# Kernel tuning notes

Measured on AMD Instinct MI355X. Metric: run time of the kernel, lower is better.

The kernel has to match this reference:

```python
import jax, jax.numpy as jnp
import numpy as np
from jax import lax

C_RED = 32
IN_CH = 256
BN_EPS = 1e-5
NORM_EPS = 1e-6


def setup_inputs() -> dict:
    key = jax.random.key(0)
    ks = jax.random.split(key, 5)
    B, H, W = 16, 64, 64
    x = jax.random.normal(ks[0], (B, IN_CH, H, W), dtype=jnp.float32)
    w_reduce = jax.random.normal(ks[1], (C_RED, IN_CH), dtype=jnp.float32) * 0.05
    bn_gamma = jnp.ones((C_RED,), dtype=jnp.float32)
    bn_beta = jnp.zeros((C_RED,), dtype=jnp.float32)
    bn_mean = jax.random.normal(ks[2], (C_RED,), dtype=jnp.float32) * 0.1
    bn_var = jax.random.uniform(ks[3], (C_RED,), dtype=jnp.float32, minval=0.5, maxval=1.5)
    # depthwise 3x3 kernel, OIHW with I=1 (groups == channels)
    dw_weight = jax.random.normal(ks[4], (C_RED, 1, 3, 3), dtype=jnp.float32) * 0.1
    scale = jnp.ones((C_RED,), dtype=jnp.float32)
    return {"x": x, "w_reduce": w_reduce, "bn_gamma": bn_gamma, "bn_beta": bn_beta,
            "bn_mean": bn_mean, "bn_var": bn_var, "dw_weight": dw_weight, "scale": scale}


def _l2_normalize(t):
    # F.normalize(p=2, dim=1, eps=1e-6): divide by max(||t||_2, eps) along channel dim
    n = jnp.sqrt(jnp.sum(t * t, axis=1, keepdims=True))
    return t / jnp.maximum(n, NORM_EPS)


def reference(x, w_reduce, bn_gamma, bn_beta, bn_mean, bn_var, dw_weight, scale):
    # 1x1 reduce conv (no bias)
    z = jnp.einsum('bihw,oi->bohw', x, w_reduce)
    # BatchNorm2d (inference: running stats)
    inv = bn_gamma / jnp.sqrt(bn_var + BN_EPS)
    z = z * inv[None, :, None, None] + (bn_beta - bn_mean * inv)[None, :, None, None]
    z = jax.nn.relu(z)
    # SpiralTwist: depthwise 3x3 conv (SAME) then per-channel scale
    z_tw = lax.conv_general_dilated(
        z, dw_weight, window_strides=(1, 1), padding='SAME',
        feature_group_count=C_RED,
        dimension_numbers=('NCHW', 'OIHW', 'NCHW'))
    z_tw = z_tw * scale[None, :, None, None]
    z_norm = _l2_normalize(z)
    z_tw_norm = _l2_normalize(z_tw)
    # upper-triangular channel pairs (i <= j)
    idx_i, idx_j = np.triu_indices(C_RED, k=0)
    pair = z_norm[:, idx_i] * z_tw_norm[:, idx_j]  # [B, C*(C+1)/2, H, W]
    return jnp.concatenate([z_norm, pair], axis=1)
```

## Files before the change

kernel.cpp:

```cpp
#include <hip/hip_runtime.h>
#include <hip/hip_bf16.h>
#include <stdint.h>

#define HW   4096
#define CIN  256
#define CR   32
#define COUT 560

__global__ __launch_bounds__(256) void k_conv1x1(
    const float* __restrict__ x,
    const float* __restrict__ wr,
    const float* __restrict__ gamma,
    const float* __restrict__ beta,
    const float* __restrict__ mean,
    const float* __restrict__ var,
    float* __restrict__ z)
{
    __shared__ __align__(16) float wlds[CR * CIN];
    const int tid = threadIdx.x;
    {
        const float4* wr4 = (const float4*)wr;
        float4* wl4 = (float4*)wlds;
        #pragma unroll
        for (int k = 0; k < 8; ++k) wl4[tid + k * 256] = wr4[tid + k * 256];
    }
    __syncthreads();

    const int og   = tid >> 6;
    const int lane = tid & 63;
    const int g0 = blockIdx.x * 256 + lane * 4;
    const int b = g0 >> 12;
    const int p = g0 & 4095;
    const float* xb = x + ((((size_t)b) * CIN) << 12) + p;
    const int ob = og * 8;

    float4 acc[8];
    #pragma unroll
    for (int o = 0; o < 8; ++o) acc[o] = make_float4(0.f, 0.f, 0.f, 0.f);

    for (int i4 = 0; i4 < 64; ++i4) {
        float4 xv0 = *(const float4*)(xb + ((size_t)(i4 * 4 + 0) << 12));
        float4 xv1 = *(const float4*)(xb + ((size_t)(i4 * 4 + 1) << 12));
        float4 xv2 = *(const float4*)(xb + ((size_t)(i4 * 4 + 2) << 12));
        float4 xv3 = *(const float4*)(xb + ((size_t)(i4 * 4 + 3) << 12));
        #pragma unroll
        for (int o = 0; o < 8; ++o) {
            float4 wv = *(const float4*)&wlds[(ob + o) * 256 + i4 * 4];
            acc[o].x = fmaf(xv0.x, wv.x, acc[o].x);
            acc[o].y = fmaf(xv0.y, wv.x, acc[o].y);
            acc[o].z = fmaf(xv0.z, wv.x, acc[o].z);
            acc[o].w = fmaf(xv0.w, wv.x, acc[o].w);
            acc[o].x = fmaf(xv1.x, wv.y, acc[o].x);
            acc[o].y = fmaf(xv1.y, wv.y, acc[o].y);
            acc[o].z = fmaf(xv1.z, wv.y, acc[o].z);
            acc[o].w = fmaf(xv1.w, wv.y, acc[o].w);
            acc[o].x = fmaf(xv2.x, wv.z, acc[o].x);
            acc[o].y = fmaf(xv2.y, wv.z, acc[o].y);
            acc[o].z = fmaf(xv2.z, wv.z, acc[o].z);
            acc[o].w = fmaf(xv2.w, wv.z, acc[o].w);
            acc[o].x = fmaf(xv3.x, wv.w, acc[o].x);
            acc[o].y = fmaf(xv3.y, wv.w, acc[o].y);
            acc[o].z = fmaf(xv3.z, wv.w, acc[o].z);
            acc[o].w = fmaf(xv3.w, wv.w, acc[o].w);
        }
    }

    #pragma unroll
    for (int o = 0; o < 8; ++o) {
        const int oc = ob + o;
        const float inv = gamma[oc] / sqrtf(var[oc] + 1e-5f);
        const float bia = beta[oc] - mean[oc] * inv;
        float4 r;
        r.x = fmaxf(fmaf(acc[o].x, inv, bia), 0.f);
        r.y = fmaxf(fmaf(acc[o].y, inv, bia), 0.f);
        r.z = fmaxf(fmaf(acc[o].z, inv, bia), 0.f);
        r.w = fmaxf(fmaf(acc[o].w, inv, bia), 0.f);
        *(float4*)(z + ((((size_t)b) * CR + oc) << 12) + p) = r;
    }
}

__global__ __launch_bounds__(256) void k_twist(
    const float* __restrict__ z,
    const float* __restrict__ dww,
    const float* __restrict__ scl,
    float* __restrict__ out)
{
    __shared__ float dml[CR * 9];
    __shared__ float sc[CR];
    const int tid = threadIdx.x;
    for (int t = tid; t < CR * 9; t += 256) dml[t] = dww[t];
    if (tid < CR) sc[tid] = scl[tid];
    __syncthreads();

    const int g = blockIdx.x * 256 + tid;
    const int b = g >> 12;
    const int p = g & 4095;
    const int h = p >> 6;
    const int w = p & 63;
    const float* zb = z + (((size_t)b * CR) << 12);

    float zc[CR], tw[CR];
    float s1 = 0.f, s2 = 0.f;
    #pragma unroll
    for (int c = 0; c < CR; ++c) {
        const float* zp = zb + ((size_t)c << 12);
        float acc = 0.f;
        float center = 0.f;
        #pragma unroll
        for (int dy = 0; dy < 3; ++dy) {
            const int hy = h + dy - 1;
            const bool rok = ((unsigned)hy) < 64u;
            #pragma unroll
            for (int dx = 0; dx < 3; ++dx) {
                const int wx = w + dx - 1;
                const bool ok = rok && (((unsigned)wx) < 64u);
                float v = 0.f;
                if (ok) v = zp[(hy << 6) + wx];
                if (dy == 1 && dx == 1) center = v;
                acc = fmaf(v, dml[c * 9 + dy * 3 + dx], acc);
            }
        }
        const float t = acc * sc[c];
        zc[c] = center;
        tw[c] = t;
        s1 = fmaf(center, center, s1);
        s2 = fmaf(t, t, s2);
    }
    const float rn1 = 1.0f / fmaxf(sqrtf(s1), 1e-6f);
    const float rn2 = 1.0f / fmaxf(sqrtf(s2), 1e-6f);
    #pragma unroll
    for (int c = 0; c < CR; ++c) { zc[c] *= rn1; tw[c] *= rn2; }

    float* op = out + (((size_t)b * COUT) << 12) + p;
    #pragma unroll
    for (int c = 0; c < CR; ++c) op[(size_t)c << 12] = zc[c];

    float* pp = op + ((size_t)CR << 12);
    #pragma unroll
    for (int i = 0; i < CR; ++i) {
        const float a = zc[i];
        #pragma unroll
        for (int j = i; j < CR; ++j) {
            *pp = a * tw[j];
            pp += HW;
        }
    }
}

extern "C" void kernel_launch(void* const* d_in, const int* in_sizes, int n_in,
                              void* d_out, int out_size, void* d_ws, size_t ws_size,
                              hipStream_t stream) {
    const float* x     = (const float*)d_in[0];
    const float* wr    = (const float*)d_in[1];
    const float* gamma = (const float*)d_in[2];
    const float* beta  = (const float*)d_in[3];
    const float* mean  = (const float*)d_in[4];
    const float* var   = (const float*)d_in[5];
    const float* dww   = (const float*)d_in[6];
    const float* scl   = (const float*)d_in[7];
    float* z = (float*)d_ws;
    float* out = (float*)d_out;

    hipLaunchKernelGGL(k_conv1x1, dim3(256), dim3(256), 0, stream,
                       x, wr, gamma, beta, mean, var, z);
    hipLaunchKernelGGL(k_twist, dim3(256), dim3(256), 0, stream,
                       z, dww, scl, out);
}
```

Baseline: 276.1 us.

## Split conv and twist work across more blocks with channel-group wave partitioning

The 1x1 conv now has each thread handle one pixel instead of four, with weights read from global memory through wave-uniform scalar loads in place of the LDS copy, and the grid grows fourfold. The twist kernel splits its 32 channels across four waves, reduces the norm partial sums through LDS, stages normalized values in LDS, and interleaves output rows across the waves. This is meant to raise occupancy and parallelism, since the old 256-block grids underfilled the GPU. In exchange it adds LDS traffic and barriers, and the conv kernel loses its float4 vectorized loads.

```diff
diff --git a/kernel.cpp b/kernel.cpp
--- a/kernel.cpp
+++ b/kernel.cpp
@@ -16,66 +16,37 @@
     const float* __restrict__ var,
     float* __restrict__ z)
 {
-    __shared__ __align__(16) float wlds[CR * CIN];
     const int tid = threadIdx.x;
-    {
-        const float4* wr4 = (const float4*)wr;
-        float4* wl4 = (float4*)wlds;
+    const int og  = __builtin_amdgcn_readfirstlane(tid >> 6);
+    const int g0  = blockIdx.x * 64 + (tid & 63);
+    const int b   = g0 >> 12;
+    const int p   = g0 & 4095;
+
+    const float* xb = x + ((((size_t)b) * CIN) << 12) + p;
+    const float* wp = wr + (size_t)og * 8 * CIN;
+
+    float acc[8] = {0.f,0.f,0.f,0.f,0.f,0.f,0.f,0.f};
+
+    for (int cc = 0; cc < 16; ++cc) {
+        float xv[16];
         #pragma unroll
-        for (int k = 0; k < 8; ++k) wl4[tid + k * 256] = wr4[tid + k * 256];
-    }
-    __syncthreads();
-
-    const int og   = tid >> 6;
-    const int lane = tid & 63;
-    const int g0 = blockIdx.x * 256 + lane * 4;
-    const int b = g0 >> 12;
-    const int p = g0 & 4095;
-    const float* xb = x + ((((size_t)b) * CIN) << 12) + p;
-    const int ob = og * 8;
-
-    float4 acc[8];
-    #pragma unroll
-    for (int o = 0; o < 8; ++o) acc[o] = make_float4(0.f, 0.f, 0.f, 0.f);
-
-    for (int i4 = 0; i4 < 64; ++i4) {
-        float4 xv0 = *(const float4*)(xb + ((size_t)(i4 * 4 + 0) << 12));
-        float4 xv1 = *(const float4*)(xb + ((size_t)(i4 * 4 + 1) << 12));
-        float4 xv2 = *(const float4*)(xb + ((size_t)(i4 * 4 + 2) << 12));
-        float4 xv3 = *(const float4*)(xb + ((size_t)(i4 * 4 + 3) << 12));
+        for (int k = 0; k < 16; ++k)
+            xv[k] = xb[((size_t)(cc * 16 + k)) << 12];
         #pragma unroll
         for (int o = 0; o < 8; ++o) {
-            float4 wv = *(const float4*)&wlds[(ob + o) * 256 + i4 * 4];
-            acc[o].x = fmaf(xv0.x, wv.x, acc[o].x);
-            acc[o].y = fmaf(xv0.y, wv.x, acc[o].y);
-            acc[o].z = fmaf(xv0.z, wv.x, acc[o].z);
-            acc[o].w = fmaf(xv0.w, wv.x, acc[o].w);
-            acc[o].x = fmaf(xv1.x, wv.y, acc[o].x);
-            acc[o].y = fmaf(xv1.y, wv.y, acc[o].y);
-            acc[o].z = fmaf(xv1.z, wv.y, acc[o].z);
-            acc[o].w = fmaf(xv1.w, wv.y, acc[o].w);
-            acc[o].x = fmaf(xv2.x, wv.z, acc[o].x);
-            acc[o].y = fmaf(xv2.y, wv.z, acc[o].y);
-            acc[o].z = fmaf(xv2.z, wv.z, acc[o].z);
-            acc[o].w = fmaf(xv2.w, wv.z, acc[o].w);
-            acc[o].x = fmaf(xv3.x, wv.w, acc[o].x);
-            acc[o].y = fmaf(xv3.y, wv.w, acc[o].y);
-            acc[o].z = fmaf(xv3.z, wv.w, acc[o].z);
-            acc[o].w = fmaf(xv3.w, wv.w, acc[o].w);
+            #pragma unroll
+            for (int k = 0; k < 16; ++k)
+                acc[o] = fmaf(xv[k], wp[o * CIN + cc * 16 + k], acc[o]);
         }
     }
 
     #pragma unroll
     for (int o = 0; o < 8; ++o) {
-        const int oc = ob + o;
+        const int oc = og * 8 + o;
         const float inv = gamma[oc] / sqrtf(var[oc] + 1e-5f);
         const float bia = beta[oc] - mean[oc] * inv;
-        float4 r;
-        r.x = fmaxf(fmaf(acc[o].x, inv, bia), 0.f);
-        r.y = fmaxf(fmaf(acc[o].y, inv, bia), 0.f);
-        r.z = fmaxf(fmaf(acc[o].z, inv, bia), 0.f);
-        r.w = fmaxf(fmaf(acc[o].w, inv, bia), 0.f);
-        *(float4*)(z + ((((size_t)b) * CR + oc) << 12) + p) = r;
+        z[((((size_t)b) * CR + oc) << 12) + p] =
+            fmaxf(fmaf(acc[o], inv, bia), 0.f);
     }
 }
 
@@ -87,32 +58,38 @@
 {
     __shared__ float dml[CR * 9];
     __shared__ float sc[CR];
+    __shared__ float ps1[4 * 64];
+    __shared__ float ps2[4 * 64];
+    __shared__ float znl[CR * 64];
+    __shared__ float twl[CR * 64];
+
     const int tid = threadIdx.x;
     for (int t = tid; t < CR * 9; t += 256) dml[t] = dww[t];
     if (tid < CR) sc[tid] = scl[tid];
     __syncthreads();
 
-    const int g = blockIdx.x * 256 + tid;
-    const int b = g >> 12;
-    const int p = g & 4095;
-    const int h = p >> 6;
-    const int w = p & 63;
+    const int cg  = __builtin_amdgcn_readfirstlane(tid >> 6);
+    const int px  = tid & 63;
+    const int g0  = blockIdx.x * 64;
+    const int b   = g0 >> 12;
+    const int p0  = g0 & 4095;
+    const int h   = p0 >> 6;
     const float* zb = z + (((size_t)b * CR) << 12);
 
-    float zc[CR], tw[CR];
+    float zc[8], tw[8];
     float s1 = 0.f, s2 = 0.f;
     #pragma unroll
-    for (int c = 0; c < CR; ++c) {
+    for (int k = 0; k < 8; ++k) {
+        const int c = cg * 8 + k;
         const float* zp = zb + ((size_t)c << 12);
-        float acc = 0.f;
-        float center = 0.f;
+        float acc = 0.f, center = 0.f;
         #pragma unroll
         for (int dy = 0; dy < 3; ++dy) {
             const int hy = h + dy - 1;
             const bool rok = ((unsigned)hy) < 64u;
             #pragma unroll
             for (int dx = 0; dx < 3; ++dx) {
-                const int wx = w + dx - 1;
+                const int wx = px + dx - 1;
                 const bool ok = rok && (((unsigned)wx) < 64u);
                 float v = 0.f;
                 if (ok) v = zp[(hy << 6) + wx];
@@ -121,28 +98,39 @@
             }
         }
         const float t = acc * sc[c];
-        zc[c] = center;
-        tw[c] = t;
+        zc[k] = center; tw[k] = t;
         s1 = fmaf(center, center, s1);
         s2 = fmaf(t, t, s2);
     }
-    const float rn1 = 1.0f / fmaxf(sqrtf(s1), 1e-6f);
-    const float rn2 = 1.0f / fmaxf(sqrtf(s2), 1e-6f);
+    ps1[cg * 64 + px] = s1;
+    ps2[cg * 64 + px] = s2;
+    __syncthreads();
+    const float t1 = ps1[px] + ps1[64 + px] + ps1[128 + px] + ps1[192 + px];
+    const float t2 = ps2[px] + ps2[64 + px] + ps2[128 + px] + ps2[192 + px];
+    const float rn1 = 1.0f / fmaxf(sqrtf(t1), 1e-6f);
+    const float rn2 = 1.0f / fmaxf(sqrtf(t2), 1e-6f);
     #pragma unroll
-    for (int c = 0; c < CR; ++c) { zc[c] *= rn1; tw[c] *= rn2; }
+    for (int k = 0; k < 8; ++k) {
+        znl[(cg * 8 + k) * 64 + px] = zc[k] * rn1;
+        twl[(cg * 8 + k) * 64 + px] = tw[k] * rn2;
+    }
+    __syncthreads();
 
-    float* op = out + (((size_t)b * COUT) << 12) + p;
+    float* outb = out + (((size_t)b * COUT) << 12) + p0 + px;
     #pragma unroll
-    for (int c = 0; c < CR; ++c) op[(size_t)c << 12] = zc[c];
-
-    float* pp = op + ((size_t)CR << 12);
-    #pragma unroll
-    for (int i = 0; i < CR; ++i) {
-        const float a = zc[i];
+    for (int P = 0; P < 32; ++P)
+        if ((P & 3) == cg)
+            outb[(size_t)P << 12] = znl[P * 64 + px];
+    {
+        int P = 32;
         #pragma unroll
-        for (int j = i; j < CR; ++j) {
-            *pp = a * tw[j];
-            pp += HW;
+        for (int i = 0; i < CR; ++i) {
+            #pragma unroll
+            for (int j = i; j < CR; ++j) {
+                if ((P & 3) == cg)
+                    outb[(size_t)P << 12] = znl[i * 64 + px] * twl[j * 64 + px];
+                ++P;
+            }
         }
     }
 }
@@ -161,8 +149,8 @@
     float* z = (float*)d_ws;
     float* out = (float*)d_out;
 
-    hipLaunchKernelGGL(k_conv1x1, dim3(256), dim3(256), 0, stream,
+    hipLaunchKernelGGL(k_conv1x1, dim3(1024), dim3(256), 0, stream,
                        x, wr, gamma, beta, mean, var, z);
-    hipLaunchKernelGGL(k_twist, dim3(256), dim3(256), 0, stream,
+    hipLaunchKernelGGL(k_twist, dim3(1024), dim3(256), 0, stream,
                        z, dww, scl, out);
 }
```

After: 240.0 us. 13.1% less time.
